# Performance work log

Measured on AMD Instinct MI355X. Metric: run time of the kernel, lower is better.

## Reference

```python
import jax, jax.numpy as jnp
import numpy as np

N_EMBD = 1024
N_HEAD = 16

def setup_inputs() -> dict:
    key = jax.random.key(0)
    ks = jax.random.split(key, 5)
    s = 0.02
    x = jax.random.normal(ks[0], (4, 2048, N_EMBD), dtype=jnp.float32)
    W_attn = jax.random.normal(ks[1], (N_EMBD, 3 * N_EMBD), dtype=jnp.float32) * s
    b_attn = jnp.zeros((3 * N_EMBD,), dtype=jnp.float32)
    W_proj = jax.random.normal(ks[2], (N_EMBD, N_EMBD), dtype=jnp.float32) * s
    b_proj = jnp.zeros((N_EMBD,), dtype=jnp.float32)
    return {"x": x, "W_attn": W_attn, "b_attn": b_attn, "W_proj": W_proj, "b_proj": b_proj}

def reference(x, W_attn, b_attn, W_proj, b_proj):
    B, T, C = x.shape
    H = N_HEAD
    Dh = C // H
    qkv = x @ W_attn + b_attn                      # [B,T,3C]
    q, k, v = jnp.split(qkv, 3, axis=2)
    # [B,T,C] -> [B,H,T,Dh]
    q = q.reshape(B, T, H, Dh).transpose(0, 2, 1, 3)
    k = k.reshape(B, T, H, Dh).transpose(0, 2, 1, 3)
    v = v.reshape(B, T, H, Dh).transpose(0, 2, 1, 3)
    scale = 1.0 / jnp.sqrt(jnp.asarray(Dh, dtype=x.dtype))
    att = jnp.einsum('bhqd,bhkd->bhqk', q, k) * scale   # [B,H,T,T]
    causal = jnp.tril(jnp.ones((T, T), dtype=bool))
    att = jnp.where(causal[None, None], att, jnp.asarray(-jnp.inf, dtype=att.dtype))
    att = jax.nn.softmax(att, axis=-1)
    out = jnp.einsum('bhqk,bhkd->bhqd', att, v)          # [B,H,T,Dh]
    out = out.transpose(0, 2, 1, 3).reshape(B, T, C)
    return out @ W_proj + b_proj
```

## Files before the change

### kernel.cpp

```cpp
#include <hip/hip_runtime.h>
#include <hip/hip_bf16.h>
#include <cstdint>

typedef unsigned short u16;
typedef __attribute__((ext_vector_type(8))) short bf16x8;
typedef __attribute__((ext_vector_type(4))) float f32x4;

#define AS1 __attribute__((address_space(1)))
#define AS3 __attribute__((address_space(3)))

#define QSCALE_CONST 0.18033688011112042f
#define SMAX_CONST 8.0f

__device__ __forceinline__ u16 f2bf(float f) {
  union { float f; unsigned u; } v; v.f = f;
  unsigned u = v.u;
  return (u16)((u + 0x7fffu + ((u >> 16) & 1u)) >> 16);
}

__device__ __forceinline__ void gload_lds16(const void* g, const void* l) {
  __builtin_amdgcn_global_load_lds(
      (const AS1 unsigned int*)(uintptr_t)g,
      (AS3 unsigned int*)(unsigned int)(uintptr_t)l,
      16, 0, 0);
}

__global__ __launch_bounds__(256) void cast_bf16_kernel(
    const float* __restrict__ in, u16* __restrict__ out, int n) {
  int i = (blockIdx.x * 256 + threadIdx.x) * 4;
  if (i >= n) return;
  float4 f = *(const float4*)(in + i);
  ushort4 o;
  o.x = f2bf(f.x); o.y = f2bf(f.y); o.z = f2bf(f.z); o.w = f2bf(f.w);
  *(ushort4*)(out + i) = o;
}

__global__ __launch_bounds__(256) void transpose_cast_kernel(
    const float* __restrict__ in, u16* __restrict__ outT, int R, int C) {
  __shared__ float tile[32][33];
  const int c0 = blockIdx.x << 5, r0 = blockIdx.y << 5;
  const int x = threadIdx.x & 31, y = threadIdx.x >> 5;
#pragma unroll
  for (int yy = y; yy < 32; yy += 8)
    tile[yy][x] = in[(size_t)(r0 + yy) * C + c0 + x];
  __syncthreads();
#pragma unroll
  for (int yy = y; yy < 32; yy += 8)
    outT[(size_t)(c0 + yy) * R + r0 + x] = f2bf(tile[x][yy]);
}

__global__ __launch_bounds__(512, 2) void gemm256_kernel(
    const u16* __restrict__ A, const u16* __restrict__ Bt,
    const float* __restrict__ bias, u16* __restrict__ Cmat,
    int M, int N, int K, int qcols) {
  __shared__ __attribute__((aligned(16))) u16 As[3][256 * 32];
  __shared__ __attribute__((aligned(16))) u16 Bs[3][256 * 32];

  const int nbn = N >> 8;
  const int nwg = (M >> 8) * nbn;
  int bid = blockIdx.x;
  if ((nwg & 7) == 0) {
    int cpx = nwg >> 3;
    bid = (bid & 7) * cpx + (bid >> 3);
  }
  const int bm = bid / nbn, bn = bid % nbn;

  const int tid = threadIdx.x;
  const int lane = tid & 63, wave = tid >> 6;
  const int g = lane >> 4, l15 = lane & 15;
  const int wm = wave >> 2, wn = wave & 3;

  const u16* Abase = A + (size_t)(bm << 8) * K;
  const u16* Bbase = Bt + (size_t)(bn << 8) * K;

  const int c0_ = tid, c1_ = 512 + tid;
  const int r0_ = c0_ >> 2, r1_ = c1_ >> 2;
  const size_t soff0 = (size_t)r0_ * K + ((c0_ & 3) ^ (r0_ & 3)) * 8;
  const size_t soff1 = (size_t)r1_ * K + ((c1_ & 3) ^ (r1_ & 3)) * 8;
  const int doff0 = c0_ * 8, doff1 = c1_ * 8;

  auto stageA = [&](int buf, int k0) {
    gload_lds16(Abase + k0 + soff0, As[buf] + doff0);
    gload_lds16(Abase + k0 + soff1, As[buf] + doff1);
  };
  auto stageB = [&](int buf, int k0) {
    gload_lds16(Bbase + k0 + soff0, Bs[buf] + doff0);
    gload_lds16(Bbase + k0 + soff1, Bs[buf] + doff1);
  };

  f32x4 zero = {0.f, 0.f, 0.f, 0.f};
  f32x4 acc[8][4];
#pragma unroll
  for (int i = 0; i < 8; ++i)
#pragma unroll
    for (int j = 0; j < 4; ++j) acc[i][j] = zero;

  const int NT = K >> 5;
  stageA(0, 0); stageB(0, 0);
  stageA(1, 32); stageB(1, 32);
  asm volatile("s_waitcnt vmcnt(4)" ::: "memory");
  __builtin_amdgcn_s_barrier();
  __builtin_amdgcn_sched_barrier(0);

#pragma unroll 1
  for (int kt = 0; kt < NT; ++kt) {
    const int cur = kt % 3, nxt = (kt + 2) % 3;
    const char* Ab = (const char*)As[cur];
    const char* Bb = (const char*)Bs[cur];

    bf16x8 af[4], bfr[4];
#pragma unroll
    for (int i = 0; i < 4; ++i) {
      int ra = wm * 128 + i * 16 + l15;
      af[i] = *(const bf16x8*)(Ab + ra * 64 + ((g ^ (ra & 3)) << 4));
    }
#pragma unroll
    for (int j = 0; j < 4; ++j) {
      int rb = wn * 64 + j * 16 + l15;
      bfr[j] = *(const bf16x8*)(Bb + rb * 64 + ((g ^ (rb & 3)) << 4));
    }
    if (kt + 2 < NT) stageA(nxt, (kt + 2) << 5);
    __builtin_amdgcn_s_barrier();
    asm volatile("s_waitcnt lgkmcnt(0)" ::: "memory");
    __builtin_amdgcn_sched_barrier(0);
    __builtin_amdgcn_s_setprio(1);
#pragma unroll
    for (int i = 0; i < 4; ++i)
#pragma unroll
      for (int j = 0; j < 4; ++j)
        acc[i][j] = __builtin_amdgcn_mfma_f32_16x16x32_bf16(af[i], bfr[j], acc[i][j], 0, 0, 0);
    __builtin_amdgcn_s_setprio(0);
    __builtin_amdgcn_s_barrier();
    __builtin_amdgcn_sched_barrier(0);

    bf16x8 ag[4];
#pragma unroll
    for (int i = 0; i < 4; ++i) {
      int ra = wm * 128 + (i + 4) * 16 + l15;
      ag[i] = *(const bf16x8*)(Ab + ra * 64 + ((g ^ (ra & 3)) << 4));
    }
    if (kt + 2 < NT) stageB(nxt, (kt + 2) << 5);
    __builtin_amdgcn_s_barrier();
    asm volatile("s_waitcnt lgkmcnt(0)" ::: "memory");
    __builtin_amdgcn_sched_barrier(0);
    __builtin_amdgcn_s_setprio(1);
#pragma unroll
    for (int i = 0; i < 4; ++i)
#pragma unroll
      for (int j = 0; j < 4; ++j)
        acc[i + 4][j] = __builtin_amdgcn_mfma_f32_16x16x32_bf16(ag[i], bfr[j], acc[i + 4][j], 0, 0, 0);
    __builtin_amdgcn_s_setprio(0);
    if (kt < NT - 2)       asm volatile("s_waitcnt vmcnt(4)" ::: "memory");
    else if (kt == NT - 2) asm volatile("s_waitcnt vmcnt(0)" ::: "memory");
    __builtin_amdgcn_s_barrier();
    __builtin_amdgcn_sched_barrier(0);
  }

#pragma unroll
  for (int i = 0; i < 8; ++i) {
    int row0 = (bm << 8) + wm * 128 + i * 16 + g * 4;
#pragma unroll
    for (int j = 0; j < 4; ++j) {
      int col = (bn << 8) + wn * 64 + j * 16 + l15;
      float bv = bias[col];
      const bool qc = col < qcols;
#pragma unroll
      for (int r = 0; r < 4; ++r) {
        float v = acc[i][j][r] + bv;
        if (qc) v *= QSCALE_CONST;
        Cmat[(size_t)(row0 + r) * N + col] = f2bf(v);
      }
    }
  }
}

template <typename OutT>
__global__ __launch_bounds__(256, 3) void gemm_bf16_kernel(
    const u16* __restrict__ A, const u16* __restrict__ Bt,
    const float* __restrict__ bias, OutT* __restrict__ Cmat,
    int M, int N, int K, int qcols) {
  __shared__ __attribute__((aligned(16))) u16 As[3][128 * 32];
  __shared__ __attribute__((aligned(16))) u16 Bs[3][128 * 32];

  const int nbn = N >> 7;
  const int nwg = (M >> 7) * nbn;
  int bid = blockIdx.x;
  if ((nwg & 7) == 0) {
    int cpx = nwg >> 3;
    bid = (bid & 7) * cpx + (bid >> 3);
  }
  const int bm = bid / nbn, bn = bid % nbn;

  const int tid = threadIdx.x;
  const int lane = tid & 63, wave = tid >> 6;
  const int g = lane >> 4, l15 = lane & 15;
  const int wrow = (wave >> 1) << 6, wcol = (wave & 1) << 6;

  const u16* Abase = A + (size_t)(bm << 7) * K;
  const u16* Bbase = Bt + (size_t)(bn << 7) * K;

  const int c0_ = wave * 64 + lane, c1_ = 256 + c0_;
  const int row0_ = c0_ >> 2, row1_ = c1_ >> 2;
  const size_t soff0 = (size_t)row0_ * K + ((c0_ & 3) ^ (row0_ & 3)) * 8;
  const size_t soff1 = (size_t)row1_ * K + ((c1_ & 3) ^ (row1_ & 3)) * 8;
  const int doff0 = c0_ * 8, doff1 = c1_ * 8;

  auto stage = [&](int buf, int k0) {
    gload_lds16(Abase + k0 + soff0, As[buf] + doff0);
    gload_lds16(Bbase + k0 + soff0, Bs[buf] + doff0);
    gload_lds16(Abase + k0 + soff1, As[buf] + doff1);
    gload_lds16(Bbase + k0 + soff1, Bs[buf] + doff1);
  };

  f32x4 zero = {0.f, 0.f, 0.f, 0.f};
  f32x4 acc[4][4];
#pragma unroll
  for (int i = 0; i < 4; ++i)
#pragma unroll
    for (int j = 0; j < 4; ++j) acc[i][j] = zero;

  const int NT = K >> 5;
  stage(0, 0);
  stage(1, 32);
#pragma unroll 1
  for (int kt = 0; kt < NT; ++kt) {
    const int cur = kt % 3;
    asm volatile("s_waitcnt lgkmcnt(0)" ::: "memory");
    __builtin_amdgcn_sched_barrier(0);
    if (kt < NT - 1) asm volatile("s_waitcnt vmcnt(4)" ::: "memory");
    else             asm volatile("s_waitcnt vmcnt(0)" ::: "memory");
    __builtin_amdgcn_s_barrier();
    if (kt + 2 < NT) stage((kt + 2) % 3, (kt + 2) << 5);

    const char* Ab = (const char*)As[cur];
    const char* Bb = (const char*)Bs[cur];
    bf16x8 af[4], bfr[4];
#pragma unroll
    for (int i = 0; i < 4; ++i) {
      int ra = wrow + i * 16 + l15;
      af[i] = *(const bf16x8*)(Ab + ra * 64 + ((g * 16) ^ ((ra & 3) << 4)));
      int rb = wcol + i * 16 + l15;
      bfr[i] = *(const bf16x8*)(Bb + rb * 64 + ((g * 16) ^ ((rb & 3) << 4)));
    }
#pragma unroll
    for (int i = 0; i < 4; ++i)
#pragma unroll
      for (int j = 0; j < 4; ++j)
        acc[i][j] = __builtin_amdgcn_mfma_f32_16x16x32_bf16(af[i], bfr[j], acc[i][j], 0, 0, 0);
  }

#pragma unroll
  for (int i = 0; i < 4; ++i) {
    int row0 = (bm << 7) + wrow + i * 16 + g * 4;
#pragma unroll
    for (int j = 0; j < 4; ++j) {
      int col = (bn << 7) + wcol + j * 16 + l15;
      float bv = bias[col];
      const bool qc = col < qcols;
#pragma unroll
      for (int r = 0; r < 4; ++r) {
        float v = acc[i][j][r] + bv;
        if (qc) v *= QSCALE_CONST;
        size_t idx = (size_t)(row0 + r) * N + col;
        if constexpr (sizeof(OutT) == 2)
          ((u16*)Cmat)[idx] = f2bf(v);
        else
          ((float*)Cmat)[idx] = v;
      }
    }
  }
}

__global__ __launch_bounds__(256, 2) void attn_kernel(
    const u16* __restrict__ qkv, u16* __restrict__ aout) {
  __shared__ __attribute__((aligned(16))) char KsB[2][8192];
  __shared__ __attribute__((aligned(16))) char VtB[2][8192];
  __shared__ __attribute__((aligned(16))) char PbB[4][4096];

  const int bh = blockIdx.x;
  const int b = bh >> 4, h = bh & 15;
  const int tid = threadIdx.x, lane = tid & 63, wave = tid >> 6;
  const int g = lane >> 4, l15 = lane & 15;

  const u16* qbase = qkv + (size_t)b * 2048 * 3072 + h * 64;
  const u16* kbase = qbase + 1024;
  const u16* vbase = qbase + 2048;

  const int krow0 = tid >> 3;
  const int ksc = (tid & 7) ^ (krow0 & 7);
  const size_t ksrc0 = (size_t)krow0 * 3072 + ksc * 8;
  const size_t ksrc1 = ksrc0 + (size_t)32 * 3072;
  const int vp_ = tid >> 3, vdh = tid & 7;
  const size_t vsrc = (size_t)(2 * vp_) * 3072 + vdh * 8;
  const int vkc = vp_ >> 2, vofs = (vp_ & 3) << 2;

  char* pb = PbB[wave];
  const f32x4 sinit = {-SMAX_CONST, -SMAX_CONST, -SMAX_CONST, -SMAX_CONST};
  f32x4 zero = {0.f, 0.f, 0.f, 0.f};

#pragma unroll 1
  for (int jj = 0; jj < 2; ++jj) {
    const int j = jj ? (15 - blockIdx.y) : blockIdx.y;
    const int q0 = j << 7;
    const int qrow = q0 + wave * 32;
    const int nt = 2 * j + 2;

    bf16x8 qfA[2], qfB[2];
#pragma unroll
    for (int kf = 0; kf < 2; ++kf) {
      qfA[kf] = *(const bf16x8*)(qbase + (size_t)(qrow + l15) * 3072 + kf * 32 + g * 8);
      qfB[kf] = *(const bf16x8*)(qbase + (size_t)(qrow + 16 + l15) * 3072 + kf * 32 + g * 8);
    }

    float lsumA = 0.f, lsumB = 0.f;
    f32x4 oA[4], oB[4];
#pragma unroll
    for (int d = 0; d < 4; ++d) { oA[d] = zero; oB[d] = zero; }

    gload_lds16(kbase + ksrc0, KsB[0] + wave * 1024);
    gload_lds16(kbase + ksrc1, KsB[0] + 4096 + wave * 1024);
    {
      bf16x8 v0 = *(const bf16x8*)(vbase + vsrc);
      bf16x8 v1 = *(const bf16x8*)(vbase + vsrc + 3072);
      char* vb = VtB[0];
#pragma unroll
      for (int q = 0; q < 8; ++q) {
        int d = vdh * 8 + q;
        int sig = q ^ vdh;
        unsigned pack = (unsigned)(u16)v0[q] | ((unsigned)(u16)v1[q] << 16);
        *(unsigned*)(vb + d * 128 + ((vkc ^ sig) << 4) + vofs) = pack;
      }
    }

    bf16x8 nv0, nv1;
#pragma unroll 1
    for (int t = 0; t < nt; ++t) {
      const int cur = t & 1;
      const int kv0 = t << 6;
      const bool pre = (t + 1 < nt);
      __syncthreads();

      if (pre) {
        const size_t nxt = (size_t)(t + 1) * 196608;
        gload_lds16(kbase + nxt + ksrc0, KsB[cur ^ 1] + wave * 1024);
        gload_lds16(kbase + nxt + ksrc1, KsB[cur ^ 1] + 4096 + wave * 1024);
        nv0 = *(const bf16x8*)(vbase + nxt + vsrc);
        nv1 = *(const bf16x8*)(vbase + nxt + vsrc + 3072);
      }

      if (qrow + 31 >= kv0) {
        const char* ks = KsB[cur];
        f32x4 sA[4], sB[4];
#pragma unroll
        for (int n = 0; n < 4; ++n) { sA[n] = sinit; sB[n] = sinit; }
#pragma unroll
        for (int kf = 0; kf < 2; ++kf)
#pragma unroll
          for (int n = 0; n < 4; ++n) {
            int row = n * 16 + l15;
            bf16x8 kfr = *(const bf16x8*)(ks + row * 128 + (((kf * 4 + g) ^ (row & 7)) << 4));
            sA[n] = __builtin_amdgcn_mfma_f32_16x16x32_bf16(kfr, qfA[kf], sA[n], 0, 0, 0);
            sB[n] = __builtin_amdgcn_mfma_f32_16x16x32_bf16(kfr, qfB[kf], sB[n], 0, 0, 0);
          }

        const int kvb = kv0 + g * 4;
        if (kv0 + 63 > qrow) {
          const int qgA = qrow + l15;
#pragma unroll
          for (int n = 0; n < 4; ++n)
#pragma unroll
            for (int r = 0; r < 4; ++r)
              if (kvb + n * 16 + r > qgA) sA[n][r] = -1e30f;
        }
        if (kv0 + 63 > qrow + 16) {
          const int qgB = qrow + 16 + l15;
#pragma unroll
          for (int n = 0; n < 4; ++n)
#pragma unroll
            for (int r = 0; r < 4; ++r)
              if (kvb + n * 16 + r > qgB) sB[n][r] = -1e30f;
        }

        float rsA = 0.f, rsB = 0.f;
#pragma unroll
        for (int n = 0; n < 4; ++n)
#pragma unroll
          for (int r = 0; r < 4; ++r) {
            float pA = __builtin_amdgcn_exp2f(sA[n][r]);
            float pB = __builtin_amdgcn_exp2f(sB[n][r]);
            sA[n][r] = pA; rsA += pA;
            sB[n][r] = pB; rsB += pB;
          }
        lsumA += rsA; lsumB += rsB;

#pragma unroll
        for (int n = 0; n < 4; ++n) {
          uint2 wA, wB;
          asm("v_cvt_pk_bf16_f32 %0, %1, %2" : "=v"(wA.x) : "v"(sA[n][0]), "v"(sA[n][1]));
          asm("v_cvt_pk_bf16_f32 %0, %1, %2" : "=v"(wA.y) : "v"(sA[n][2]), "v"(sA[n][3]));
          asm("v_cvt_pk_bf16_f32 %0, %1, %2" : "=v"(wB.x) : "v"(sB[n][0]), "v"(sB[n][1]));
          asm("v_cvt_pk_bf16_f32 %0, %1, %2" : "=v"(wB.y) : "v"(sB[n][2]), "v"(sB[n][3]));
          int c = n * 2 + (g >> 1);
          int boff = (((c ^ (l15 & 7)) << 4) | ((g & 1) << 3)) + l15 * 128;
          *(uint2*)(pb + boff) = wA;
          *(uint2*)(pb + 2048 + boff) = wB;
        }

        const char* vt = VtB[cur];
        bf16x8 pfA[2], pfB[2];
#pragma unroll
        for (int kf = 0; kf < 2; ++kf) {
          int poff = l15 * 128 + (((kf * 4 + g) ^ (l15 & 7)) << 4);
          pfA[kf] = *(const bf16x8*)(pb + poff);
          pfB[kf] = *(const bf16x8*)(pb + 2048 + poff);
        }
#pragma unroll
        for (int kf = 0; kf < 2; ++kf)
#pragma unroll
          for (int d = 0; d < 4; ++d) {
            int dr = d * 16 + l15;
            int sig = (dr & 7) ^ ((dr >> 3) & 7);
            bf16x8 vf = *(const bf16x8*)(vt + dr * 128 + (((kf * 4 + g) ^ sig) << 4));
            oA[d] = __builtin_amdgcn_mfma_f32_16x16x32_bf16(pfA[kf], vf, oA[d], 0, 0, 0);
            oB[d] = __builtin_amdgcn_mfma_f32_16x16x32_bf16(pfB[kf], vf, oB[d], 0, 0, 0);
          }
      }

      if (pre) {
        char* vb = VtB[cur ^ 1];
#pragma unroll
        for (int q = 0; q < 8; ++q) {
          int d = vdh * 8 + q;
          int sig = q ^ vdh;
          unsigned pack = (unsigned)(u16)nv0[q] | ((unsigned)(u16)nv1[q] << 16);
          *(unsigned*)(vb + d * 128 + ((vkc ^ sig) << 4) + vofs) = pack;
        }
      }
    }

    lsumA += __shfl_xor(lsumA, 16); lsumA += __shfl_xor(lsumA, 32);
    lsumB += __shfl_xor(lsumB, 16); lsumB += __shfl_xor(lsumB, 32);
    float invA[4], invB[4];
#pragma unroll
    for (int r = 0; r < 4; ++r) {
      invA[r] = __builtin_amdgcn_rcpf(__shfl(lsumA, g * 4 + r));
      invB[r] = __builtin_amdgcn_rcpf(__shfl(lsumB, g * 4 + r));
    }
    const size_t obase = (size_t)(b * 2048 + qrow) * 1024 + h * 64;
#pragma unroll
    for (int d = 0; d < 4; ++d)
#pragma unroll
      for (int r = 0; r < 4; ++r) {
        aout[obase + (size_t)(g * 4 + r) * 1024 + d * 16 + l15] = f2bf(oA[d][r] * invA[r]);
        aout[obase + (size_t)(16 + g * 4 + r) * 1024 + d * 16 + l15] = f2bf(oB[d][r] * invB[r]);
      }
  }
}

extern "C" void kernel_launch(void* const* d_in, const int* in_sizes, int n_in,
                              void* d_out, int out_size, void* d_ws, size_t ws_size,
                              hipStream_t stream) {
  const float* x      = (const float*)d_in[0];
  const float* W_attn = (const float*)d_in[1];
  const float* b_attn = (const float*)d_in[2];
  const float* W_proj = (const float*)d_in[3];
  const float* b_proj = (const float*)d_in[4];
  float* out = (float*)d_out;

  char* ws = (char*)d_ws;
  u16* xb   = (u16*)(ws);
  u16* Wat  = (u16*)(ws + (size_t)16 * 1024 * 1024);
  u16* Wpt  = (u16*)(ws + (size_t)22 * 1024 * 1024);
  u16* qkv  = (u16*)(ws + (size_t)24 * 1024 * 1024);
  u16* aout = (u16*)(ws + (size_t)72 * 1024 * 1024);

  cast_bf16_kernel<<<8192, 256, 0, stream>>>(x, xb, 8388608);
  transpose_cast_kernel<<<dim3(96, 32), 256, 0, stream>>>(W_attn, Wat, 1024, 3072);
  transpose_cast_kernel<<<dim3(32, 32), 256, 0, stream>>>(W_proj, Wpt, 1024, 1024);
  gemm256_kernel<<<384, 512, 0, stream>>>(xb, Wat, b_attn, qkv, 8192, 3072, 1024, 1024);
  attn_kernel<<<dim3(64, 8), 256, 0, stream>>>(qkv, aout);
  gemm_bf16_kernel<float><<<512, 256, 0, stream>>>(aout, Wpt, b_proj, out, 8192, 1024, 1024, 0);
}
```

Measured before the change: 170.5 us.

## Restructure GEMM pipeline to double-buffered 64-wide K tiles with new LDS swizzle

The QKV/projection GEMM moves from a triple-buffered 32-wide K pipeline to a double-buffered scheme. Each buffer holds two 32-wide sub-slabs, so each loop iteration covers 64 of K, and the next tile's sub-slabs are prefetched during the current compute phases. The LDS swizzle changes from row&3 to (row>>1)&3 to reduce bank conflicts on the 16-byte fragment reads. Barrier placement and vmcnt waits are reworked to fit the new schedule. The goal is fewer barriers per unit of K and better load/compute overlap, but the prefetch distance is shorter and the wait logic is more delicate.

Measured after the change: 166.2 us. 1.03x faster.

```diff
diff --git a/kernel.cpp b/kernel.cpp
--- a/kernel.cpp
+++ b/kernel.cpp
@@ -53,8 +53,7 @@
     const u16* __restrict__ A, const u16* __restrict__ Bt,
     const float* __restrict__ bias, u16* __restrict__ Cmat,
     int M, int N, int K, int qcols) {
-  __shared__ __attribute__((aligned(16))) u16 As[3][256 * 32];
-  __shared__ __attribute__((aligned(16))) u16 Bs[3][256 * 32];
+  __shared__ __attribute__((aligned(16))) u16 L[2][4][8192];
 
   const int nbn = N >> 8;
   const int nwg = (M >> 8) * nbn;
@@ -73,19 +72,18 @@
   const u16* Abase = A + (size_t)(bm << 8) * K;
   const u16* Bbase = Bt + (size_t)(bn << 8) * K;
 
-  const int c0_ = tid, c1_ = 512 + tid;
-  const int r0_ = c0_ >> 2, r1_ = c1_ >> 2;
-  const size_t soff0 = (size_t)r0_ * K + ((c0_ & 3) ^ (r0_ & 3)) * 8;
-  const size_t soff1 = (size_t)r1_ * K + ((c1_ & 3) ^ (r1_ & 3)) * 8;
-  const int doff0 = c0_ * 8, doff1 = c1_ * 8;
-
-  auto stageA = [&](int buf, int k0) {
-    gload_lds16(Abase + k0 + soff0, As[buf] + doff0);
-    gload_lds16(Abase + k0 + soff1, As[buf] + doff1);
-  };
-  auto stageB = [&](int buf, int k0) {
-    gload_lds16(Bbase + k0 + soff0, Bs[buf] + doff0);
-    gload_lds16(Bbase + k0 + soff1, Bs[buf] + doff1);
+  const int cA = tid, rA = cA >> 2;
+  const int cB = 512 + tid, rB = cB >> 2;
+  const size_t soff0 = (size_t)rA * K + (((cA & 3) ^ ((rA >> 1) & 3)) * 8);
+  const size_t soff1 = (size_t)rB * K + (((cB & 3) ^ ((rB >> 1) & 3)) * 8);
+  const int doff0 = cA * 8, doff1 = cB * 8;
+
+  auto stageS = [&](int buf, int s, int kt) {
+    const size_t kof = (size_t)kt * 64 + s * 32;
+    gload_lds16(Abase + kof + soff0, &L[buf][s][0] + doff0);
+    gload_lds16(Abase + kof + soff1, &L[buf][s][0] + doff1);
+    gload_lds16(Bbase + kof + soff0, &L[buf][2 + s][0] + doff0);
+    gload_lds16(Bbase + kof + soff1, &L[buf][2 + s][0] + doff1);
   };
 
   f32x4 zero = {0.f, 0.f, 0.f, 0.f};
@@ -95,32 +93,35 @@
 #pragma unroll
     for (int j = 0; j < 4; ++j) acc[i][j] = zero;
 
-  const int NT = K >> 5;
-  stageA(0, 0); stageB(0, 0);
-  stageA(1, 32); stageB(1, 32);
+  const int NT = K >> 6;
+
+  stageS(0, 0, 0);
+  stageS(0, 1, 0);
   asm volatile("s_waitcnt vmcnt(4)" ::: "memory");
   __builtin_amdgcn_s_barrier();
   __builtin_amdgcn_sched_barrier(0);
 
 #pragma unroll 1
   for (int kt = 0; kt < NT; ++kt) {
-    const int cur = kt % 3, nxt = (kt + 2) % 3;
-    const char* Ab = (const char*)As[cur];
-    const char* Bb = (const char*)Bs[cur];
-
-    bf16x8 af[4], bfr[4];
+    const int cbuf = kt & 1, nbuf = cbuf ^ 1;
+    const bool more = (kt + 1 < NT);
+    const char* A0 = (const char*)&L[cbuf][0][0];
+    const char* A1 = (const char*)&L[cbuf][1][0];
+    const char* B0 = (const char*)&L[cbuf][2][0];
+    const char* B1 = (const char*)&L[cbuf][3][0];
+
+    bf16x8 af[4], bf[4];
 #pragma unroll
     for (int i = 0; i < 4; ++i) {
       int ra = wm * 128 + i * 16 + l15;
-      af[i] = *(const bf16x8*)(Ab + ra * 64 + ((g ^ (ra & 3)) << 4));
+      af[i] = *(const bf16x8*)(A0 + ra * 64 + ((g ^ ((ra >> 1) & 3)) << 4));
     }
 #pragma unroll
     for (int j = 0; j < 4; ++j) {
       int rb = wn * 64 + j * 16 + l15;
-      bfr[j] = *(const bf16x8*)(Bb + rb * 64 + ((g ^ (rb & 3)) << 4));
-    }
-    if (kt + 2 < NT) stageA(nxt, (kt + 2) << 5);
-    __builtin_amdgcn_s_barrier();
+      bf[j] = *(const bf16x8*)(B0 + rb * 64 + ((g ^ ((rb >> 1) & 3)) << 4));
+    }
+    if (more) stageS(nbuf, 0, kt + 1);
     asm volatile("s_waitcnt lgkmcnt(0)" ::: "memory");
     __builtin_amdgcn_sched_barrier(0);
     __builtin_amdgcn_s_setprio(1);
@@ -128,19 +129,41 @@
     for (int i = 0; i < 4; ++i)
 #pragma unroll
       for (int j = 0; j < 4; ++j)
-        acc[i][j] = __builtin_amdgcn_mfma_f32_16x16x32_bf16(af[i], bfr[j], acc[i][j], 0, 0, 0);
+        acc[i][j] = __builtin_amdgcn_mfma_f32_16x16x32_bf16(af[i], bf[j], acc[i][j], 0, 0, 0);
     __builtin_amdgcn_s_setprio(0);
     __builtin_amdgcn_s_barrier();
     __builtin_amdgcn_sched_barrier(0);
 
-    bf16x8 ag[4];
 #pragma unroll
     for (int i = 0; i < 4; ++i) {
       int ra = wm * 128 + (i + 4) * 16 + l15;
-      ag[i] = *(const bf16x8*)(Ab + ra * 64 + ((g ^ (ra & 3)) << 4));
-    }
-    if (kt + 2 < NT) stageB(nxt, (kt + 2) << 5);
+      af[i] = *(const bf16x8*)(A0 + ra * 64 + ((g ^ ((ra >> 1) & 3)) << 4));
+    }
+    asm volatile("s_waitcnt lgkmcnt(0)" ::: "memory");
+    __builtin_amdgcn_sched_barrier(0);
+    __builtin_amdgcn_s_setprio(1);
+#pragma unroll
+    for (int i = 0; i < 4; ++i)
+#pragma unroll
+      for (int j = 0; j < 4; ++j)
+        acc[i + 4][j] = __builtin_amdgcn_mfma_f32_16x16x32_bf16(af[i], bf[j], acc[i + 4][j], 0, 0, 0);
+    __builtin_amdgcn_s_setprio(0);
+    if (more) asm volatile("s_waitcnt vmcnt(4)" ::: "memory");
+    else      asm volatile("s_waitcnt vmcnt(0)" ::: "memory");
     __builtin_amdgcn_s_barrier();
+    __builtin_amdgcn_sched_barrier(0);
+
+#pragma unroll
+    for (int i = 0; i < 4; ++i) {
+      int ra = wm * 128 + i * 16 + l15;
+      af[i] = *(const bf16x8*)(A1 + ra * 64 + ((g ^ ((ra >> 1) & 3)) << 4));
+    }
+#pragma unroll
+    for (int j = 0; j < 4; ++j) {
+      int rb = wn * 64 + j * 16 + l15;
+      bf[j] = *(const bf16x8*)(B1 + rb * 64 + ((g ^ ((rb >> 1) & 3)) << 4));
+    }
+    if (more) stageS(nbuf, 1, kt + 1);
     asm volatile("s_waitcnt lgkmcnt(0)" ::: "memory");
     __builtin_amdgcn_sched_barrier(0);
     __builtin_amdgcn_s_setprio(1);
@@ -148,10 +171,27 @@
     for (int i = 0; i < 4; ++i)
 #pragma unroll
       for (int j = 0; j < 4; ++j)
-        acc[i + 4][j] = __builtin_amdgcn_mfma_f32_16x16x32_bf16(ag[i], bfr[j], acc[i + 4][j], 0, 0, 0);
+        acc[i][j] = __builtin_amdgcn_mfma_f32_16x16x32_bf16(af[i], bf[j], acc[i][j], 0, 0, 0);
     __builtin_amdgcn_s_setprio(0);
-    if (kt < NT - 2)       asm volatile("s_waitcnt vmcnt(4)" ::: "memory");
-    else if (kt == NT - 2) asm volatile("s_waitcnt vmcnt(0)" ::: "memory");
+    __builtin_amdgcn_s_barrier();
+    __builtin_amdgcn_sched_barrier(0);
+
+#pragma unroll
+    for (int i = 0; i < 4; ++i) {
+      int ra = wm * 128 + (i + 4) * 16 + l15;
+      af[i] = *(const bf16x8*)(A1 + ra * 64 + ((g ^ ((ra >> 1) & 3)) << 4));
+    }
+    asm volatile("s_waitcnt lgkmcnt(0)" ::: "memory");
+    __builtin_amdgcn_sched_barrier(0);
+    __builtin_amdgcn_s_setprio(1);
+#pragma unroll
+    for (int i = 0; i < 4; ++i)
+#pragma unroll
+      for (int j = 0; j < 4; ++j)
+        acc[i + 4][j] = __builtin_amdgcn_mfma_f32_16x16x32_bf16(af[i], bf[j], acc[i + 4][j], 0, 0, 0);
+    __builtin_amdgcn_s_setprio(0);
+    if (more) asm volatile("s_waitcnt vmcnt(4)" ::: "memory");
+    else      asm volatile("s_waitcnt vmcnt(0)" ::: "memory");
     __builtin_amdgcn_s_barrier();
     __builtin_amdgcn_sched_barrier(0);
   }
```

## Shrink QKV GEMM tile to 128x256 and load attention K fragments directly from global

Applied to the files above, without the earlier changes.

The QKV projection GEMM moves from a 256x256 tile with a triple-buffered K=32 pipeline to a 128x256 tile with a double-buffered K=64 pipeline (two 32-wide substages) and a new swizzle. This doubles the workgroup count to 768. The attention kernel drops its LDS staging of K and reads K fragments directly from global memory per lane. That frees LDS so occupancy can rise to 4 blocks per CU. The risks are lower arithmetic intensity in the GEMM and uncoalesced, repeated global reads of K in attention.

Result: slower. 299.3 us (median of 2 runs) (+75.6%).

```diff
diff --git a/kernel.cpp b/kernel.cpp
--- a/kernel.cpp
+++ b/kernel.cpp
@@ -49,15 +49,15 @@
     outT[(size_t)(c0 + yy) * R + r0 + x] = f2bf(tile[x][yy]);
 }
 
-__global__ __launch_bounds__(512, 2) void gemm256_kernel(
+__global__ __launch_bounds__(512, 2) void gemm1_kernel(
     const u16* __restrict__ A, const u16* __restrict__ Bt,
     const float* __restrict__ bias, u16* __restrict__ Cmat,
     int M, int N, int K, int qcols) {
-  __shared__ __attribute__((aligned(16))) u16 As[3][256 * 32];
-  __shared__ __attribute__((aligned(16))) u16 Bs[3][256 * 32];
+  __shared__ __attribute__((aligned(16))) u16 LA[2][2][128 * 32];
+  __shared__ __attribute__((aligned(16))) u16 LB[2][2][256 * 32];
 
   const int nbn = N >> 8;
-  const int nwg = (M >> 8) * nbn;
+  const int nwg = (M >> 7) * nbn;
   int bid = blockIdx.x;
   if ((nwg & 7) == 0) {
     int cpx = nwg >> 3;
@@ -70,95 +70,77 @@
   const int g = lane >> 4, l15 = lane & 15;
   const int wm = wave >> 2, wn = wave & 3;
 
-  const u16* Abase = A + (size_t)(bm << 8) * K;
+  const u16* Abase = A + (size_t)(bm << 7) * K;
   const u16* Bbase = Bt + (size_t)(bn << 8) * K;
 
-  const int c0_ = tid, c1_ = 512 + tid;
-  const int r0_ = c0_ >> 2, r1_ = c1_ >> 2;
-  const size_t soff0 = (size_t)r0_ * K + ((c0_ & 3) ^ (r0_ & 3)) * 8;
-  const size_t soff1 = (size_t)r1_ * K + ((c1_ & 3) ^ (r1_ & 3)) * 8;
-  const int doff0 = c0_ * 8, doff1 = c1_ * 8;
-
-  auto stageA = [&](int buf, int k0) {
-    gload_lds16(Abase + k0 + soff0, As[buf] + doff0);
-    gload_lds16(Abase + k0 + soff1, As[buf] + doff1);
+  const int rA = tid >> 2;
+  const size_t aoff = (size_t)rA * K + (((tid & 3) ^ ((rA >> 1) & 3)) * 8);
+  const int rB0 = tid >> 2;
+  const size_t boff0 = (size_t)rB0 * K + (((tid & 3) ^ ((rB0 >> 1) & 3)) * 8);
+  const int cB1 = 512 + tid, rB1 = cB1 >> 2;
+  const size_t boff1 = (size_t)rB1 * K + (((cB1 & 3) ^ ((rB1 >> 1) & 3)) * 8);
+
+  auto stageG = [&](int buf, int s, int kt) {
+    const size_t kof = (size_t)kt * 64 + s * 32;
+    gload_lds16(Abase + kof + aoff, &LA[buf][s][0] + tid * 8);
+    gload_lds16(Bbase + kof + boff0, &LB[buf][s][0] + tid * 8);
+    gload_lds16(Bbase + kof + boff1, &LB[buf][s][0] + (512 + tid) * 8);
   };
-  auto stageB = [&](int buf, int k0) {
-    gload_lds16(Bbase + k0 + soff0, Bs[buf] + doff0);
-    gload_lds16(Bbase + k0 + soff1, Bs[buf] + doff1);
-  };
 
   f32x4 zero = {0.f, 0.f, 0.f, 0.f};
-  f32x4 acc[8][4];
-#pragma unroll
-  for (int i = 0; i < 8; ++i)
+  f32x4 acc[4][4];
+#pragma unroll
+  for (int i = 0; i < 4; ++i)
 #pragma unroll
     for (int j = 0; j < 4; ++j) acc[i][j] = zero;
 
-  const int NT = K >> 5;
-  stageA(0, 0); stageB(0, 0);
-  stageA(1, 32); stageB(1, 32);
-  asm volatile("s_waitcnt vmcnt(4)" ::: "memory");
+  const int NT = K >> 6;
+
+  stageG(0, 0, 0);
+  stageG(0, 1, 0);
+  asm volatile("s_waitcnt vmcnt(3)" ::: "memory");
   __builtin_amdgcn_s_barrier();
   __builtin_amdgcn_sched_barrier(0);
 
 #pragma unroll 1
   for (int kt = 0; kt < NT; ++kt) {
-    const int cur = kt % 3, nxt = (kt + 2) % 3;
-    const char* Ab = (const char*)As[cur];
-    const char* Bb = (const char*)Bs[cur];
-
-    bf16x8 af[4], bfr[4];
-#pragma unroll
-    for (int i = 0; i < 4; ++i) {
-      int ra = wm * 128 + i * 16 + l15;
-      af[i] = *(const bf16x8*)(Ab + ra * 64 + ((g ^ (ra & 3)) << 4));
-    }
-#pragma unroll
-    for (int j = 0; j < 4; ++j) {
-      int rb = wn * 64 + j * 16 + l15;
-      bfr[j] = *(const bf16x8*)(Bb + rb * 64 + ((g ^ (rb & 3)) << 4));
-    }
-    if (kt + 2 < NT) stageA(nxt, (kt + 2) << 5);
-    __builtin_amdgcn_s_barrier();
-    asm volatile("s_waitcnt lgkmcnt(0)" ::: "memory");
-    __builtin_amdgcn_sched_barrier(0);
-    __builtin_amdgcn_s_setprio(1);
-#pragma unroll
-    for (int i = 0; i < 4; ++i)
-#pragma unroll
-      for (int j = 0; j < 4; ++j)
-        acc[i][j] = __builtin_amdgcn_mfma_f32_16x16x32_bf16(af[i], bfr[j], acc[i][j], 0, 0, 0);
-    __builtin_amdgcn_s_setprio(0);
-    __builtin_amdgcn_s_barrier();
-    __builtin_amdgcn_sched_barrier(0);
-
-    bf16x8 ag[4];
-#pragma unroll
-    for (int i = 0; i < 4; ++i) {
-      int ra = wm * 128 + (i + 4) * 16 + l15;
-      ag[i] = *(const bf16x8*)(Ab + ra * 64 + ((g ^ (ra & 3)) << 4));
-    }
-    if (kt + 2 < NT) stageB(nxt, (kt + 2) << 5);
-    __builtin_amdgcn_s_barrier();
-    asm volatile("s_waitcnt lgkmcnt(0)" ::: "memory");
-    __builtin_amdgcn_sched_barrier(0);
-    __builtin_amdgcn_s_setprio(1);
-#pragma unroll
-    for (int i = 0; i < 4; ++i)
-#pragma unroll
-      for (int j = 0; j < 4; ++j)
-        acc[i + 4][j] = __builtin_amdgcn_mfma_f32_16x16x32_bf16(ag[i], bfr[j], acc[i + 4][j], 0, 0, 0);
-    __builtin_amdgcn_s_setprio(0);
-    if (kt < NT - 2)       asm volatile("s_waitcnt vmcnt(4)" ::: "memory");
-    else if (kt == NT - 2) asm volatile("s_waitcnt vmcnt(0)" ::: "memory");
-    __builtin_amdgcn_s_barrier();
-    __builtin_amdgcn_sched_barrier(0);
-  }
-
-#pragma unroll
-  for (int i = 0; i < 8; ++i) {
-    int row0 = (bm << 8) + wm * 128 + i * 16 + g * 4;
+    const int cbuf = kt & 1, nbuf = cbuf ^ 1;
+    const bool more = (kt + 1 < NT);
+#pragma unroll
+    for (int s = 0; s < 2; ++s) {
+      const char* Ab = (const char*)&LA[cbuf][s][0];
+      const char* Bb = (const char*)&LB[cbuf][s][0];
+      bf16x8 af[4], bfr[4];
+#pragma unroll
+      for (int i = 0; i < 4; ++i) {
+        int ra = wm * 64 + i * 16 + l15;
+        af[i] = *(const bf16x8*)(Ab + ra * 64 + ((g ^ ((ra >> 1) & 3)) << 4));
+      }
+#pragma unroll
+      for (int j = 0; j < 4; ++j) {
+        int rb = wn * 64 + j * 16 + l15;
+        bfr[j] = *(const bf16x8*)(Bb + rb * 64 + ((g ^ ((rb >> 1) & 3)) << 4));
+      }
+      if (more) stageG(nbuf, s, kt + 1);
+      asm volatile("s_waitcnt lgkmcnt(0)" ::: "memory");
+      __builtin_amdgcn_sched_barrier(0);
+      __builtin_amdgcn_s_setprio(1);
+#pragma unroll
+      for (int i = 0; i < 4; ++i)
+#pragma unroll
+        for (int j = 0; j < 4; ++j)
+          acc[i][j] = __builtin_amdgcn_mfma_f32_16x16x32_bf16(af[i], bfr[j], acc[i][j], 0, 0, 0);
+      __builtin_amdgcn_s_setprio(0);
+      if (more)            asm volatile("s_waitcnt vmcnt(3)" ::: "memory");
+      else if (s == 0)     asm volatile("s_waitcnt vmcnt(0)" ::: "memory");
+      __builtin_amdgcn_s_barrier();
+      __builtin_amdgcn_sched_barrier(0);
+    }
+  }
+
+#pragma unroll
+  for (int i = 0; i < 4; ++i) {
+    int row0 = (bm << 7) + wm * 64 + i * 16 + g * 4;
 #pragma unroll
     for (int j = 0; j < 4; ++j) {
       int col = (bn << 8) + wn * 64 + j * 16 + l15;
@@ -271,9 +253,8 @@
   }
 }
 
-__global__ __launch_bounds__(256, 2) void attn_kernel(
+__global__ __launch_bounds__(256, 4) void attn_kernel(
     const u16* __restrict__ qkv, u16* __restrict__ aout) {
-  __shared__ __attribute__((aligned(16))) char KsB[2][8192];
   __shared__ __attribute__((aligned(16))) char VtB[2][8192];
   __shared__ __attribute__((aligned(16))) char PbB[4][4096];
 
@@ -285,11 +266,8 @@
   const u16* qbase = qkv + (size_t)b * 2048 * 3072 + h * 64;
   const u16* kbase = qbase + 1024;
   const u16* vbase = qbase + 2048;
-
-  const int krow0 = tid >> 3;
-  const int ksc = (tid & 7) ^ (krow0 & 7);
-  const size_t ksrc0 = (size_t)krow0 * 3072 + ksc * 8;
-  const size_t ksrc1 = ksrc0 + (size_t)32 * 3072;
+  const u16* klane = kbase + (size_t)l15 * 3072 + g * 8;
+
   const int vp_ = tid >> 3, vdh = tid & 7;
   const size_t vsrc = (size_t)(2 * vp_) * 3072 + vdh * 8;
   const int vkc = vp_ >> 2, vofs = (vp_ & 3) << 2;
@@ -317,8 +295,6 @@
 #pragma unroll
     for (int d = 0; d < 4; ++d) { oA[d] = zero; oB[d] = zero; }
 
-    gload_lds16(kbase + ksrc0, KsB[0] + wave * 1024);
-    gload_lds16(kbase + ksrc1, KsB[0] + 4096 + wave * 1024);
     {
       bf16x8 v0 = *(const bf16x8*)(vbase + vsrc);
       bf16x8 v1 = *(const bf16x8*)(vbase + vsrc + 3072);
@@ -342,14 +318,11 @@
 
       if (pre) {
         const size_t nxt = (size_t)(t + 1) * 196608;
-        gload_lds16(kbase + nxt + ksrc0, KsB[cur ^ 1] + wave * 1024);
-        gload_lds16(kbase + nxt + ksrc1, KsB[cur ^ 1] + 4096 + wave * 1024);
         nv0 = *(const bf16x8*)(vbase + nxt + vsrc);
         nv1 = *(const bf16x8*)(vbase + nxt + vsrc + 3072);
       }
 
       if (qrow + 31 >= kv0) {
-        const char* ks = KsB[cur];
         f32x4 sA[4], sB[4];
 #pragma unroll
         for (int n = 0; n < 4; ++n) { sA[n] = sinit; sB[n] = sinit; }
@@ -357,8 +330,7 @@
         for (int kf = 0; kf < 2; ++kf)
 #pragma unroll
           for (int n = 0; n < 4; ++n) {
-            int row = n * 16 + l15;
-            bf16x8 kfr = *(const bf16x8*)(ks + row * 128 + (((kf * 4 + g) ^ (row & 7)) << 4));
+            bf16x8 kfr = *(const bf16x8*)(klane + (size_t)(kv0 + n * 16) * 3072 + kf * 32);
             sA[n] = __builtin_amdgcn_mfma_f32_16x16x32_bf16(kfr, qfA[kf], sA[n], 0, 0, 0);
             sB[n] = __builtin_amdgcn_mfma_f32_16x16x32_bf16(kfr, qfB[kf], sB[n], 0, 0, 0);
           }
@@ -477,7 +449,7 @@
   cast_bf16_kernel<<<8192, 256, 0, stream>>>(x, xb, 8388608);
   transpose_cast_kernel<<<dim3(96, 32), 256, 0, stream>>>(W_attn, Wat, 1024, 3072);
   transpose_cast_kernel<<<dim3(32, 32), 256, 0, stream>>>(W_proj, Wpt, 1024, 1024);
-  gemm256_kernel<<<384, 512, 0, stream>>>(xb, Wat, b_attn, qkv, 8192, 3072, 1024, 1024);
+  gemm1_kernel<<<768, 512, 0, stream>>>(xb, Wat, b_attn, qkv, 8192, 3072, 1024, 1024);
   attn_kernel<<<dim3(64, 8), 256, 0, stream>>>(qkv, aout);
   gemm_bf16_kernel<float><<<512, 256, 0, stream>>>(aout, Wpt, b_proj, out, 8192, 1024, 1024, 0);
 }
```
